# Performance work log

Measured on AMD Instinct MI355X. Metric: run time of the kernel, lower is better.

Reference implementation:

```python
import jax, jax.numpy as jnp
import numpy as np

B, D_IN, UNITS = 8192, 4096, 4096

def setup_inputs() -> dict:
    key = jax.random.key(0)
    k1, k2 = jax.random.split(key)
    x = jax.random.normal(k1, (B, D_IN), dtype=jnp.float32)
    w = jax.random.normal(k2, (D_IN, UNITS), dtype=jnp.float32)
    b = jnp.zeros((UNITS,), dtype=jnp.float32)
    return {"x": x, "w": w, "b": b}

def reference(x, w, b):
    # Bipolar dense: sign-binarize the weights, full-precision matmul, bias, relu.
    weights = jnp.sign(w)  # values in {-1, 0, +1}; matches tf.math.sign
    out = jnp.matmul(x, weights) + b  # [B, UNITS]
    return jax.nn.relu(out)
```

## Files before the change

### kernel.cpp

```cpp
#include <hip/hip_runtime.h>
#include <hip/hip_bf16.h>
#include <stdint.h>

#define M_DIM 8192
#define N_DIM 4096
#define K_DIM 4096

typedef __attribute__((ext_vector_type(4))) int   int4v;
typedef __attribute__((ext_vector_type(4))) float floatx4;

__global__ __launch_bounds__(256) void quant_x_kernel(const float* __restrict__ x,
                                                      signed char* __restrict__ xq,
                                                      float* __restrict__ xs) {
    const int row = blockIdx.x;
    const int tid = threadIdx.x;
    const int wave = tid >> 6, lane = tid & 63;
    const float4* xr = (const float4*)(x + (size_t)row * K_DIM);

    float4 v[4];
    float m = 0.f;
    #pragma unroll
    for (int j = 0; j < 4; ++j) {
        v[j] = xr[j * 256 + tid];
        m = fmaxf(m, fmaxf(fmaxf(fabsf(v[j].x), fabsf(v[j].y)),
                           fmaxf(fabsf(v[j].z), fabsf(v[j].w))));
    }
    #pragma unroll
    for (int off = 32; off >= 1; off >>= 1) m = fmaxf(m, __shfl_down(m, off));
    __shared__ float wm[4];
    if (lane == 0) wm[wave] = m;
    __syncthreads();
    const float M = fmaxf(fmaxf(wm[0], wm[1]), fmaxf(wm[2], wm[3]));
    const float inv = M > 0.f ? 127.f / M : 0.f;
    if (tid == 0) xs[row] = M > 0.f ? M / 127.f : 0.f;

    char4* xo = (char4*)(xq + (size_t)row * K_DIM);
    #pragma unroll
    for (int j = 0; j < 4; ++j) {
        char4 q;
        q.x = (signed char)__float2int_rn(v[j].x * inv);
        q.y = (signed char)__float2int_rn(v[j].y * inv);
        q.z = (signed char)__float2int_rn(v[j].z * inv);
        q.w = (signed char)__float2int_rn(v[j].w * inv);
        xo[j * 256 + tid] = q;
    }
}

__global__ __launch_bounds__(256) void cvt_w_kernel(const float* __restrict__ w,
                                                    signed char* __restrict__ wT) {
    __shared__ signed char tile[64][68];
    const int t  = threadIdx.x;
    const int k0 = blockIdx.y * 64;
    const int n0 = blockIdx.x * 64;
    #pragma unroll
    for (int p = 0; p < 4; ++p) {
        int kk = p * 16 + (t >> 4);
        int nn = (t & 15) * 4;
        float4 v = *reinterpret_cast<const float4*>(&w[(size_t)(k0 + kk) * N_DIM + n0 + nn]);
        tile[kk][nn + 0] = v.x > 0.f ? 1 : (v.x < 0.f ? -1 : 0);
        tile[kk][nn + 1] = v.y > 0.f ? 1 : (v.y < 0.f ? -1 : 0);
        tile[kk][nn + 2] = v.z > 0.f ? 1 : (v.z < 0.f ? -1 : 0);
        tile[kk][nn + 3] = v.w > 0.f ? 1 : (v.w < 0.f ? -1 : 0);
    }
    __syncthreads();
    const int r = t >> 2;
    const int c = (t & 3) * 16;
    int4v o;
    signed char* op = (signed char*)&o;
    #pragma unroll
    for (int j = 0; j < 16; ++j) op[j] = tile[c + j][r];
    *reinterpret_cast<int4v*>(&wT[(size_t)(n0 + r) * K_DIM + k0 + c]) = o;
}

#define BM 256
#define BN 256
#define BK 64
#define NT (K_DIM / BK)

#define GLD(gsrc, ldst) __builtin_amdgcn_global_load_lds( \
    (const __attribute__((address_space(1))) unsigned int*)(gsrc), \
    (__attribute__((address_space(3))) unsigned int*)(ldst), 16, 0, 0)

__global__ __launch_bounds__(512, 2) void gemm_i8_kernel(
    const signed char* __restrict__ A,
    const signed char* __restrict__ BT,
    const float* __restrict__ xsc,
    const float* __restrict__ bias,
    float* __restrict__ C)
{
    __shared__ signed char As[2][2][128 * 64];
    __shared__ signed char Bs[3][2][128 * 64];

    const int tid  = threadIdx.x;
    const int wave = tid >> 6;
    const int lane = tid & 63;
    const int wm   = wave >> 2;
    const int wn   = wave & 3;
    const int bh   = wn >> 1;
    const int brow0 = (wn & 1) * 64;

    const int bid  = blockIdx.x;
    const int sbid = (bid & 7) * 64 + (bid >> 3);
    const int tn   = sbid & 15;
    const int tm   = sbid >> 4;
    const int bm   = tm * BM;
    const int bn   = tn * BN;

    const int srow = tid >> 2;
    const int scol = ((tid & 3) ^ ((tid >> 3) & 3)) * 16;

    const int laneRow = (lane & 15) * 64;
    const int colX = ((lane >> 4) * 16) ^ (((lane >> 1) & 3) << 4);

    int4v acc[8][4] = {};

#define STAGE_HALF(G, R0, KOFS, LDST) do { \
    GLD((G) + (size_t)((R0) + srow) * K_DIM + (KOFS) + scol, (LDST) + wave * 1024); \
  } while (0)

    STAGE_HALF(BT, bn,        0, Bs[0][0]);
    STAGE_HALF(BT, bn + 128,  0, Bs[0][1]);
    STAGE_HALF(A,  bm,        0, As[0][0]);
    STAGE_HALF(A,  bm + 128,  0, As[0][1]);
    STAGE_HALF(BT, bn,       BK, Bs[1][0]);
    STAGE_HALF(BT, bn + 128, BK, Bs[1][1]);
    asm volatile("s_waitcnt vmcnt(2)" ::: "memory");
    __builtin_amdgcn_s_barrier();

    int4v a[4];
    int4v a2[4];
    int4v b[4];

    int brd = 0;
    int bst = 2;

    for (int t = 0; t < NT; ++t) {
        const int abuf = t & 1;
        const char* Ar = (const char*)As[abuf][wm];
        const char* Br = (const char*)Bs[brd][bh];
        const int kA = (t + 1 < NT ? t + 1 : NT - 1) * BK;
        const int kB = (t + 2 < NT ? t + 2 : NT - 1) * BK;

        a[0]  = *(const int4v*)(Ar + (0*16)*64 + laneRow + colX);
        b[0]  = *(const int4v*)(Br + (brow0 +  0)*64 + laneRow + colX);
        b[1]  = *(const int4v*)(Br + (brow0 + 16)*64 + laneRow + colX);
        b[2]  = *(const int4v*)(Br + (brow0 + 32)*64 + laneRow + colX);
        b[3]  = *(const int4v*)(Br + (brow0 + 48)*64 + laneRow + colX);
        a[1]  = *(const int4v*)(Ar + (1*16)*64 + laneRow + colX);
        a[2]  = *(const int4v*)(Ar + (2*16)*64 + laneRow + colX);
        a[3]  = *(const int4v*)(Ar + (3*16)*64 + laneRow + colX);
        a2[0] = *(const int4v*)(Ar + ((64 + 0*16))*64 + laneRow + colX);
        a2[1] = *(const int4v*)(Ar + ((64 + 1*16))*64 + laneRow + colX);
        a2[2] = *(const int4v*)(Ar + ((64 + 2*16))*64 + laneRow + colX);
        a2[3] = *(const int4v*)(Ar + ((64 + 3*16))*64 + laneRow + colX);

        STAGE_HALF(A,  bm,       kA, As[abuf ^ 1][0]);
        STAGE_HALF(A,  bm + 128, kA, As[abuf ^ 1][1]);
        STAGE_HALF(BT, bn,       kB, Bs[bst][0]);
        STAGE_HALF(BT, bn + 128, kB, Bs[bst][1]);

        __builtin_amdgcn_s_setprio(1);
        #pragma unroll
        for (int mf = 0; mf < 4; ++mf)
            #pragma unroll
            for (int nf = 0; nf < 4; ++nf)
                acc[mf][nf] = __builtin_amdgcn_mfma_i32_16x16x64_i8(
                    a[mf], b[nf], acc[mf][nf], 0, 0, 0);
        #pragma unroll
        for (int mf = 0; mf < 4; ++mf)
            #pragma unroll
            for (int nf = 0; nf < 4; ++nf)
                acc[4 + mf][nf] = __builtin_amdgcn_mfma_i32_16x16x64_i8(
                    a2[mf], b[nf], acc[4 + mf][nf], 0, 0, 0);
        __builtin_amdgcn_s_setprio(0);

        asm volatile("s_waitcnt vmcnt(2)" ::: "memory");
        __builtin_amdgcn_s_barrier();

        brd = (brd == 2) ? 0 : brd + 1;
        bst = (bst == 2) ? 0 : bst + 1;
    }

    float bv[4];
    #pragma unroll
    for (int nf = 0; nf < 4; ++nf)
        bv[nf] = bias[bn + wn * 64 + nf * 16 + (lane & 15)];
    #pragma unroll
    for (int mf = 0; mf < 8; ++mf) {
        const int row0 = bm + wm * 128 + mf * 16 + (lane >> 4) * 4;
        float sr[4];
        #pragma unroll
        for (int r = 0; r < 4; ++r) sr[r] = xsc[row0 + r];
        #pragma unroll
        for (int nf = 0; nf < 4; ++nf) {
            const int col = bn + wn * 64 + nf * 16 + (lane & 15);
            float* cp = C + (size_t)row0 * N_DIM + col;
            #pragma unroll
            for (int r = 0; r < 4; ++r) {
                float v = (float)acc[mf][nf][r] * sr[r] + bv[nf];
                cp[(size_t)r * N_DIM] = v > 0.f ? v : 0.f;
            }
        }
    }
}

__global__ void naive_kernel(const float* __restrict__ x, const float* __restrict__ w,
                             const float* __restrict__ b, float* __restrict__ out) {
    __shared__ float xs[16][16];
    __shared__ float ws[16][17];
    const int row = blockIdx.y * 16 + threadIdx.y;
    const int col = blockIdx.x * 16 + threadIdx.x;
    float acc = 0.f;
    for (int k0 = 0; k0 < K_DIM; k0 += 16) {
        xs[threadIdx.y][threadIdx.x] = x[(size_t)row * K_DIM + k0 + threadIdx.x];
        float wv = w[(size_t)(k0 + threadIdx.y) * N_DIM + col];
        ws[threadIdx.y][threadIdx.x] = wv > 0.f ? 1.f : (wv < 0.f ? -1.f : 0.f);
        __syncthreads();
        #pragma unroll
        for (int kk = 0; kk < 16; ++kk) acc += xs[threadIdx.y][kk] * ws[kk][threadIdx.x];
        __syncthreads();
    }
    float v = acc + b[col];
    out[(size_t)row * N_DIM + col] = v > 0.f ? v : 0.f;
}

extern "C" void kernel_launch(void* const* d_in, const int* in_sizes, int n_in,
                              void* d_out, int out_size, void* d_ws, size_t ws_size,
                              hipStream_t stream) {
    const float* x = (const float*)d_in[0];
    const float* w = (const float*)d_in[1];
    const float* b = (const float*)d_in[2];
    float* out = (float*)d_out;

    const size_t xq_bytes = (size_t)M_DIM * K_DIM;
    const size_t wT_bytes = (size_t)K_DIM * N_DIM;
    const size_t xs_bytes = (size_t)M_DIM * sizeof(float);

    if (ws_size >= xq_bytes + wT_bytes + xs_bytes) {
        signed char* xq = (signed char*)d_ws;
        signed char* wT = (signed char*)((char*)d_ws + xq_bytes);
        float*       xs = (float*)((char*)d_ws + xq_bytes + wT_bytes);
        quant_x_kernel<<<M_DIM, 256, 0, stream>>>(x, xq, xs);
        cvt_w_kernel<<<dim3(N_DIM / 64, K_DIM / 64), 256, 0, stream>>>(w, wT);
        gemm_i8_kernel<<<(M_DIM / BM) * (N_DIM / BN), 512, 0, stream>>>(xq, wT, xs, b, out);
    } else {
        naive_kernel<<<dim3(N_DIM / 16, M_DIM / 16), dim3(16, 16), 0, stream>>>(x, w, b, out);
    }
}
```

Baseline: 186.0 us.

## Load B fragments directly from global into registers, dropping B LDS staging

Weight (B) fragments now go straight from global memory into registers, with per-lane pointers and a two-deep register double buffer, instead of being staged through a triple-buffered LDS ring. Only A is still staged in LDS, which frees shared memory and removes the B LDS reads. The loop is unrolled by two so the register buffers alternate, and launch bounds drop to one block per SM to allow more registers. The risks are exposed global-load latency on B, since only one tile of prefetch distance remains, less efficient global access patterns, and lower occupancy.

```diff
diff --git a/kernel.cpp b/kernel.cpp
--- a/kernel.cpp
+++ b/kernel.cpp
@@ -81,7 +81,7 @@
     (const __attribute__((address_space(1))) unsigned int*)(gsrc), \
     (__attribute__((address_space(3))) unsigned int*)(ldst), 16, 0, 0)
 
-__global__ __launch_bounds__(512, 2) void gemm_i8_kernel(
+__global__ __launch_bounds__(512, 1) void gemm_i8_kernel(
     const signed char* __restrict__ A,
     const signed char* __restrict__ BT,
     const float* __restrict__ xsc,
@@ -89,15 +89,12 @@
     float* __restrict__ C)
 {
     __shared__ signed char As[2][2][128 * 64];
-    __shared__ signed char Bs[3][2][128 * 64];
 
     const int tid  = threadIdx.x;
     const int wave = tid >> 6;
     const int lane = tid & 63;
     const int wm   = wave >> 2;
     const int wn   = wave & 3;
-    const int bh   = wn >> 1;
-    const int brow0 = (wn & 1) * 64;
 
     const int bid  = blockIdx.x;
     const int sbid = (bid & 7) * 64 + (bid >> 3);
@@ -112,73 +109,70 @@
     const int laneRow = (lane & 15) * 64;
     const int colX = ((lane >> 4) * 16) ^ (((lane >> 1) & 3) << 4);
 
+    const signed char* bb[4];
+    #pragma unroll
+    for (int nf = 0; nf < 4; ++nf)
+        bb[nf] = BT + (size_t)(bn + wn * 64 + nf * 16 + (lane & 15)) * K_DIM
+                    + (lane >> 4) * 16;
+
     int4v acc[8][4] = {};
-
-#define STAGE_HALF(G, R0, KOFS, LDST) do { \
-    GLD((G) + (size_t)((R0) + srow) * K_DIM + (KOFS) + scol, (LDST) + wave * 1024); \
+    int4v a[4], a2[4];
+    int4v bA[4], bB[4];
+
+#define STAGE_HALF(R0, KOFS, LDST) do { \
+    GLD(A + (size_t)((R0) + srow) * K_DIM + (KOFS) + scol, (LDST) + wave * 1024); \
   } while (0)
 
-    STAGE_HALF(BT, bn,        0, Bs[0][0]);
-    STAGE_HALF(BT, bn + 128,  0, Bs[0][1]);
-    STAGE_HALF(A,  bm,        0, As[0][0]);
-    STAGE_HALF(A,  bm + 128,  0, As[0][1]);
-    STAGE_HALF(BT, bn,       BK, Bs[1][0]);
-    STAGE_HALF(BT, bn + 128, BK, Bs[1][1]);
-    asm volatile("s_waitcnt vmcnt(2)" ::: "memory");
+#define LOAD_B(SLOT, KOFS) do { \
+    SLOT[0] = *(const int4v*)(bb[0] + (KOFS)); \
+    SLOT[1] = *(const int4v*)(bb[1] + (KOFS)); \
+    SLOT[2] = *(const int4v*)(bb[2] + (KOFS)); \
+    SLOT[3] = *(const int4v*)(bb[3] + (KOFS)); \
+  } while (0)
+
+    STAGE_HALF(bm,       0, As[0][0]);
+    STAGE_HALF(bm + 128, 0, As[0][1]);
+    LOAD_B(bA, 0);
+    LOAD_B(bB, BK);
+    asm volatile("s_waitcnt vmcnt(4)" ::: "memory");
     __builtin_amdgcn_s_barrier();
 
-    int4v a[4];
-    int4v a2[4];
-    int4v b[4];
-
-    int brd = 0;
-    int bst = 2;
-
-    for (int t = 0; t < NT; ++t) {
-        const int abuf = t & 1;
-        const char* Ar = (const char*)As[abuf][wm];
-        const char* Br = (const char*)Bs[brd][bh];
-        const int kA = (t + 1 < NT ? t + 1 : NT - 1) * BK;
-        const int kB = (t + 2 < NT ? t + 2 : NT - 1) * BK;
-
-        a[0]  = *(const int4v*)(Ar + (0*16)*64 + laneRow + colX);
-        b[0]  = *(const int4v*)(Br + (brow0 +  0)*64 + laneRow + colX);
-        b[1]  = *(const int4v*)(Br + (brow0 + 16)*64 + laneRow + colX);
-        b[2]  = *(const int4v*)(Br + (brow0 + 32)*64 + laneRow + colX);
-        b[3]  = *(const int4v*)(Br + (brow0 + 48)*64 + laneRow + colX);
-        a[1]  = *(const int4v*)(Ar + (1*16)*64 + laneRow + colX);
-        a[2]  = *(const int4v*)(Ar + (2*16)*64 + laneRow + colX);
-        a[3]  = *(const int4v*)(Ar + (3*16)*64 + laneRow + colX);
-        a2[0] = *(const int4v*)(Ar + ((64 + 0*16))*64 + laneRow + colX);
-        a2[1] = *(const int4v*)(Ar + ((64 + 1*16))*64 + laneRow + colX);
-        a2[2] = *(const int4v*)(Ar + ((64 + 2*16))*64 + laneRow + colX);
-        a2[3] = *(const int4v*)(Ar + ((64 + 3*16))*64 + laneRow + colX);
-
-        STAGE_HALF(A,  bm,       kA, As[abuf ^ 1][0]);
-        STAGE_HALF(A,  bm + 128, kA, As[abuf ^ 1][1]);
-        STAGE_HALF(BT, bn,       kB, Bs[bst][0]);
-        STAGE_HALF(BT, bn + 128, kB, Bs[bst][1]);
-
-        __builtin_amdgcn_s_setprio(1);
-        #pragma unroll
-        for (int mf = 0; mf < 4; ++mf)
-            #pragma unroll
-            for (int nf = 0; nf < 4; ++nf)
-                acc[mf][nf] = __builtin_amdgcn_mfma_i32_16x16x64_i8(
-                    a[mf], b[nf], acc[mf][nf], 0, 0, 0);
-        #pragma unroll
-        for (int mf = 0; mf < 4; ++mf)
-            #pragma unroll
-            for (int nf = 0; nf < 4; ++nf)
-                acc[4 + mf][nf] = __builtin_amdgcn_mfma_i32_16x16x64_i8(
-                    a2[mf], b[nf], acc[4 + mf][nf], 0, 0, 0);
-        __builtin_amdgcn_s_setprio(0);
-
-        asm volatile("s_waitcnt vmcnt(2)" ::: "memory");
-        __builtin_amdgcn_s_barrier();
-
-        brd = (brd == 2) ? 0 : brd + 1;
-        bst = (bst == 2) ? 0 : bst + 1;
+#define TILE_BODY(T, AR_IDX, AS_IDX, BCUR) do { \
+    const char* Ar = (const char*)As[AR_IDX][wm]; \
+    const int kA = ((T) + 1 < NT ? (T) + 1 : NT - 1) * BK; \
+    const int kB = ((T) + 2 < NT ? (T) + 2 : NT - 1) * BK; \
+    a[0]  = *(const int4v*)(Ar + (0*16)*64 + laneRow + colX); \
+    a[1]  = *(const int4v*)(Ar + (1*16)*64 + laneRow + colX); \
+    a[2]  = *(const int4v*)(Ar + (2*16)*64 + laneRow + colX); \
+    a[3]  = *(const int4v*)(Ar + (3*16)*64 + laneRow + colX); \
+    a2[0] = *(const int4v*)(Ar + ((64+0*16))*64 + laneRow + colX); \
+    a2[1] = *(const int4v*)(Ar + ((64+1*16))*64 + laneRow + colX); \
+    a2[2] = *(const int4v*)(Ar + ((64+2*16))*64 + laneRow + colX); \
+    a2[3] = *(const int4v*)(Ar + ((64+3*16))*64 + laneRow + colX); \
+    STAGE_HALF(bm,       kA, As[AS_IDX][0]); \
+    STAGE_HALF(bm + 128, kA, As[AS_IDX][1]); \
+    __builtin_amdgcn_s_setprio(1); \
+    _Pragma("unroll") \
+    for (int mf = 0; mf < 4; ++mf) \
+        _Pragma("unroll") \
+        for (int nf = 0; nf < 4; ++nf) \
+            acc[mf][nf] = __builtin_amdgcn_mfma_i32_16x16x64_i8( \
+                a[mf], BCUR[nf], acc[mf][nf], 0, 0, 0); \
+    _Pragma("unroll") \
+    for (int mf = 0; mf < 4; ++mf) \
+        _Pragma("unroll") \
+        for (int nf = 0; nf < 4; ++nf) \
+            acc[4 + mf][nf] = __builtin_amdgcn_mfma_i32_16x16x64_i8( \
+                a2[mf], BCUR[nf], acc[4 + mf][nf], 0, 0, 0); \
+    __builtin_amdgcn_s_setprio(0); \
+    LOAD_B(BCUR, kB);  \
+    asm volatile("s_waitcnt vmcnt(4)" ::: "memory"); \
+    __builtin_amdgcn_s_barrier(); \
+  } while (0)
+
+    for (int t = 0; t < NT; t += 2) {
+        TILE_BODY(t,     0, 1, bA);
+        TILE_BODY(t + 1, 1, 0, bB);
     }
 
     float bv[4];
```

Result: slower. 242.9 us (+30.6%).
